# Performance work log

Hardware: AMD Instinct MI355X
Metric: run time of the kernel (lower is better)

The kernel has to match this reference:

```python
import jax, jax.numpy as jnp
import numpy as np

N_NODES_TOTAL = 61440   # B*30
NODES = 30              # per-graph node count (forced by view(-1, 30*128))
E = 491520
IN_CH = 12
CHANS = [128, 512, 128]
KSIZE = 3
FC_OUT = 72             # 12 * 6


def setup_inputs() -> dict:
    key = jax.random.key(0)
    ks = jax.random.split(key, 24)
    d = {}
    d['x'] = jax.random.normal(ks[0], (N_NODES_TOTAL, IN_CH), dtype=jnp.float32)
    d['edge_index'] = jax.random.randint(ks[1], (2, E), 0, N_NODES_TOTAL, dtype=jnp.int64)
    # GCNConv(12, 12): PyG Linear weight [out, in] + bias
    d['gcn_w'] = jax.random.normal(ks[2], (12, 12), dtype=jnp.float32) * (1.0 / np.sqrt(12))
    d['gcn_b'] = jnp.zeros((12,), dtype=jnp.float32)
    # TCN: 3 TemporalBlocks, each uses conv1 (k=3, dilated causal) + 1x1 downsample
    in_c = IN_CH
    for i, out_c in enumerate(CHANS):
        d[f'conv_w{i}'] = jax.random.normal(ks[3 + 4 * i], (out_c, in_c, KSIZE), dtype=jnp.float32) * 0.01
        d[f'conv_b{i}'] = jnp.zeros((out_c,), dtype=jnp.float32)
        d[f'down_w{i}'] = jax.random.normal(ks[4 + 4 * i], (out_c, in_c, 1), dtype=jnp.float32) * 0.01
        d[f'down_b{i}'] = jnp.zeros((out_c,), dtype=jnp.float32)
        in_c = out_c
    d['fc_w'] = jax.random.normal(ks[20], (FC_OUT, CHANS[-1] * NODES), dtype=jnp.float32) * (1.0 / np.sqrt(CHANS[-1] * NODES))
    d['fc_b'] = jnp.zeros((FC_OUT,), dtype=jnp.float32)
    return d


def gcn_conv(x, edge_index, w, b):
    # PyG GCNConv: h = x W^T, add self-loops, sym normalize, scatter-add, + bias
    n = x.shape[0]
    h = x @ w.T
    loop = jnp.arange(n, dtype=edge_index.dtype)
    src = jnp.concatenate([edge_index[0], loop])
    dst = jnp.concatenate([edge_index[1], loop])
    deg = jax.ops.segment_sum(jnp.ones(src.shape[0], dtype=h.dtype), dst, num_segments=n)
    dinv = jnp.where(deg > 0, jax.lax.rsqrt(deg), 0.0)
    norm = dinv[src] * dinv[dst]                       # [E+N]
    out = jax.ops.segment_sum(norm[:, None] * h[src], dst, num_segments=n)
    return out + b


def causal_conv1d(x, w, b, dilation):
    # torch Conv1d(pad=(k-1)*d both sides) + Chomp1d((k-1)*d) == left-pad causal conv
    k = w.shape[-1]
    pad = (k - 1) * dilation
    y = jax.lax.conv_general_dilated(
        x, w, window_strides=(1,), padding=[(pad, 0)],
        rhs_dilation=(dilation,), dimension_numbers=('NCH', 'OIH', 'NCH'))
    return y + b[None, :, None]


def reference(x, edge_index, gcn_w, gcn_b,
              conv_w0, conv_b0, down_w0, down_b0,
              conv_w1, conv_b1, down_w1, down_b1,
              conv_w2, conv_b2, down_w2, down_b2,
              fc_w, fc_b):
    X = gcn_conv(x, edge_index, gcn_w, gcn_b)          # [B*30, 12]
    X = X.reshape(-1, NODES, IN_CH).transpose(0, 2, 1)  # [B, 12, 30]
    blocks = [(conv_w0, conv_b0, down_w0, down_b0),
              (conv_w1, conv_b1, down_w1, down_b1),
              (conv_w2, conv_b2, down_w2, down_b2)]
    for i, (cw, cb, dw, db) in enumerate(blocks):
        dil = 3 ** i
        out = jax.nn.relu(causal_conv1d(X, cw, cb, dil))
        res = causal_conv1d(X, dw, db, 1)              # 1x1 downsample (always in!=out here)
        X = jax.nn.relu(out + res)
    T = jax.nn.relu(X)                                  # [B, 128, 30]
    T = T.reshape(T.shape[0], -1)                       # [B, 3840], channel-major like torch flatten
    return T @ fc_w.T + fc_b                            # [B, 72]
```

## Files before the change

kernel.cpp:

```cpp
#include <hip/hip_runtime.h>
#include <hip/hip_bf16.h>

#define N_NODES 61440
#define NEDGE   491520
#define BATCH   2048
#define TT      30
#define C1      128
#define C2      512
#define C3      128
#define FCK     3840
#define MAXDEG  40

typedef float floatx16 __attribute__((ext_vector_type(16)));
typedef __bf16 bfrag   __attribute__((ext_vector_type(8)));

static __device__ __forceinline__ unsigned short f2bf(float f) {
    unsigned u = __float_as_uint(f);
    u = u + 0x7fffu + ((u >> 16) & 1u);
    return (unsigned short)(u >> 16);
}
static __device__ __forceinline__ unsigned cvtpk(float lo, float hi) {
    unsigned r;
    asm("v_cvt_pk_bf16_f32 %0, %1, %2" : "=v"(r) : "v"(lo), "v"(hi));
    return r;
}
static __device__ __forceinline__ bfrag ldf(const void* p) { return *(const bfrag*)p; }
#define MFMA(a, b, c) __builtin_amdgcn_mfma_f32_32x32x16_bf16(a, b, c, 0, 0, 0)

__global__ void k_edges_repack(
        const int* __restrict__ e32, int* __restrict__ cnt,
        unsigned short* __restrict__ eidx,
        const float* __restrict__ cw0, const float* __restrict__ dw0,
        const float* __restrict__ cw1, const float* __restrict__ dw1,
        const float* __restrict__ cw2, const float* __restrict__ dw2,
        const float* __restrict__ fcw,
        float* __restrict__ w0T, float* __restrict__ d0T,
        unsigned short* __restrict__ W1f, unsigned short* __restrict__ D1f,
        unsigned short* __restrict__ W2f, unsigned short* __restrict__ D2f,
        unsigned short* __restrict__ FCWf) {
    if (blockIdx.x < 1920) {
        int i = blockIdx.x * 256 + threadIdx.x;
        bool is64 = (e32[1] == 0) & (e32[3] == 0) & (e32[5] == 0) & (e32[7] == 0);
        int s, d;
        if (is64) { s = e32[2 * i]; d = e32[2 * (NEDGE + i)]; }
        else      { s = e32[i];     d = e32[NEDGE + i]; }
        int slot = atomicAdd(&cnt[d], 1);
        if (slot < MAXDEG) eidx[slot * N_NODES + d] = (unsigned short)s;
        return;
    }
    int i = (blockIdx.x - 1920) * 256 + threadIdx.x;
    if (i < 36 * 128) { int oc = i & 127, r = i >> 7; w0T[i] = cw0[oc * 36 + r]; }
    if (i < 12 * 128) { int oc = i & 127, ic = i >> 7; d0T[i] = dw0[oc * 12 + ic]; }
    if (i < 196608) {
        int pos = i & 511, f = i >> 9;
        int lane = pos >> 3, e = pos & 7;
        int oct = f & 15, q = (f >> 4) & 7, tap = f >> 7;
        int oc = oct * 32 + (lane & 31), ic = q * 16 + (lane >> 5) * 8 + e;
        W1f[i] = f2bf(cw1[(oc * 128 + ic) * 3 + tap]);
    } else if (i < 262144) {
        int j = i - 196608;
        int pos = j & 511, f = j >> 9;
        int lane = pos >> 3, e = pos & 7;
        int oct = f & 15, q = f >> 4;
        int oc = oct * 32 + (lane & 31), ic = q * 16 + (lane >> 5) * 8 + e;
        D1f[j] = f2bf(dw1[oc * 128 + ic]);
    } else if (i < 458752) {
        int j = i - 262144;
        int pos = j & 511, f = j >> 9;
        int lane = pos >> 3, e = pos & 7;
        int oct = f & 3, q = (f >> 2) & 31, tap = f >> 7;
        int oc = oct * 32 + (lane & 31), ic = q * 16 + (lane >> 5) * 8 + e;
        W2f[j] = f2bf(cw2[(oc * 512 + ic) * 3 + tap]);
    } else if (i < 524288) {
        int j = i - 458752;
        int pos = j & 511, f = j >> 9;
        int lane = pos >> 3, e = pos & 7;
        int oct = f & 3, q = f >> 2;
        int oc = oct * 32 + (lane & 31), ic = q * 16 + (lane >> 5) * 8 + e;
        D2f[j] = f2bf(dw2[oc * 512 + ic]);
    } else if (i < 892928) {
        int j = i - 524288;
        int pos = j & 511, f = j >> 9;
        int lane = pos >> 3, e = pos & 7;
        int oct = f % 3, q = f / 3;
        int o = oct * 32 + (lane & 31);
        int k = q * 16 + (lane >> 5) * 8 + e;
        float v = (o < 72) ? fcw[o * 3840 + (k & 127) * 30 + (k >> 7)] : 0.f;
        FCWf[j] = f2bf(v);
    }
}

__global__ __launch_bounds__(256) void k_block0(
        const float* __restrict__ x, const int* __restrict__ cnt,
        const unsigned short* __restrict__ eidx,
        const float* __restrict__ gw, const float* __restrict__ gb,
        const float* __restrict__ w0T, const float* __restrict__ d0T,
        const float* __restrict__ cb0, const float* __restrict__ db0,
        unsigned short* __restrict__ X1b) {
    __shared__ float wl[36 * 128];
    __shared__ float dl[12 * 128];
    __shared__ float cbl[128], dbl[128];
    __shared__ float gwl[144], gbl[12];
    __shared__ float aL[120][12];
    __shared__ float x0[4 * TT * 12];
    __shared__ __align__(16) unsigned short st[2][TT * 136];
    int tid = threadIdx.x;
    int b0 = blockIdx.x * 4;
    for (int i = tid; i < 36 * 128; i += 256) wl[i] = w0T[i];
    for (int i = tid; i < 12 * 128; i += 256) dl[i] = d0T[i];
    if (tid < 128) { cbl[tid] = cb0[tid]; dbl[tid] = db0[tid]; }
    if (tid < 144) gwl[tid] = gw[tid];
    if (tid >= 144 && tid < 156) gbl[tid - 144] = gb[tid - 144];

    {
        int th = tid & 127;
        int grp = tid >> 7;
        if (th < 120) {
            size_t n = (size_t)b0 * TT + th;
            int ne = cnt[n]; if (ne > MAXDEG) ne = MAXDEG;
            float a0 = 0.f, a1 = 0.f, a2 = 0.f, a3 = 0.f, a4 = 0.f, a5 = 0.f;
            int j = 0;
            for (; j + 4 <= ne; j += 4) {
                int s0 = eidx[(j + 0) * N_NODES + n];
                int s1 = eidx[(j + 1) * N_NODES + n];
                int s2 = eidx[(j + 2) * N_NODES + n];
                int s3 = eidx[(j + 3) * N_NODES + n];
                float di0 = rsqrtf(1.0f + (float)cnt[s0]);
                float di1 = rsqrtf(1.0f + (float)cnt[s1]);
                float di2 = rsqrtf(1.0f + (float)cnt[s2]);
                float di3 = rsqrtf(1.0f + (float)cnt[s3]);
                const float2* xp0 = (const float2*)(x + (size_t)s0 * 12 + grp * 6);
                const float2* xp1 = (const float2*)(x + (size_t)s1 * 12 + grp * 6);
                const float2* xp2 = (const float2*)(x + (size_t)s2 * 12 + grp * 6);
                const float2* xp3 = (const float2*)(x + (size_t)s3 * 12 + grp * 6);
                float2 q00 = xp0[0], q01 = xp0[1], q02 = xp0[2];
                float2 q10 = xp1[0], q11 = xp1[1], q12 = xp1[2];
                float2 q20 = xp2[0], q21 = xp2[1], q22 = xp2[2];
                float2 q30 = xp3[0], q31 = xp3[1], q32 = xp3[2];
                a0 += di0 * q00.x; a1 += di0 * q00.y;
                a2 += di0 * q01.x; a3 += di0 * q01.y;
                a4 += di0 * q02.x; a5 += di0 * q02.y;
                a0 += di1 * q10.x; a1 += di1 * q10.y;
                a2 += di1 * q11.x; a3 += di1 * q11.y;
                a4 += di1 * q12.x; a5 += di1 * q12.y;
                a0 += di2 * q20.x; a1 += di2 * q20.y;
                a2 += di2 * q21.x; a3 += di2 * q21.y;
                a4 += di2 * q22.x; a5 += di2 * q22.y;
                a0 += di3 * q30.x; a1 += di3 * q30.y;
                a2 += di3 * q31.x; a3 += di3 * q31.y;
                a4 += di3 * q32.x; a5 += di3 * q32.y;
            }
            for (; j < ne; j++) {
                int s = eidx[j * N_NODES + n];
                float di = rsqrtf(1.0f + (float)cnt[s]);
                const float2* xp = (const float2*)(x + (size_t)s * 12 + grp * 6);
                float2 p0 = xp[0], p1 = xp[1], p2 = xp[2];
                a0 += di * p0.x; a1 += di * p0.y;
                a2 += di * p1.x; a3 += di * p1.y;
                a4 += di * p2.x; a5 += di * p2.y;
            }
            float* ap = &aL[th][grp * 6];
            ap[0] = a0; ap[1] = a1; ap[2] = a2; ap[3] = a3; ap[4] = a4; ap[5] = a5;
        }
    }
    __syncthreads();

    if (tid < 120) {
        size_t n = (size_t)b0 * TT + tid;
        float di = rsqrtf(1.0f + (float)cnt[n]);
        float d2 = di * di;
        const float4* xp = (const float4*)(x + n * 12);
        float u[12];
        #pragma unroll
        for (int q = 0; q < 3; q++) {
            float4 xv = xp[q];
            u[q*4+0] = di * aL[tid][q*4+0] + d2 * xv.x;
            u[q*4+1] = di * aL[tid][q*4+1] + d2 * xv.y;
            u[q*4+2] = di * aL[tid][q*4+2] + d2 * xv.z;
            u[q*4+3] = di * aL[tid][q*4+3] + d2 * xv.w;
        }
        #pragma unroll
        for (int c = 0; c < 12; c++) {
            float acc = gbl[c];
            #pragma unroll
            for (int j = 0; j < 12; j++) acc += u[j] * gwl[c * 12 + j];
            x0[tid * 12 + c] = acc;
        }
    }
    __syncthreads();

    int oc = tid & 127, half = tid >> 7;
    float cb = cbl[oc], db = dbl[oc];
    for (int bi = 0; bi < 2; bi++) {
        int bl = bi * 2 + half;
        const float* xb = x0 + bl * (TT * 12);
        float conv[TT], res[TT];
        #pragma unroll
        for (int t = 0; t < TT; t++) { conv[t] = 0.f; res[t] = 0.f; }
        #pragma unroll
        for (int ic = 0; ic < 12; ic++) {
            float w0v = wl[(ic * 3 + 0) * 128 + oc];
            float w1v = wl[(ic * 3 + 1) * 128 + oc];
            float w2v = wl[(ic * 3 + 2) * 128 + oc];
            float dv  = dl[ic * 128 + oc];
            #pragma unroll
            for (int t = 0; t < TT; t++) {
                float xv = xb[t * 12 + ic];
                conv[t] += w2v * xv;
                if (t + 1 < TT) conv[t + 1] += w1v * xv;
                if (t + 2 < TT) conv[t + 2] += w0v * xv;
                res[t] += dv * xv;
            }
        }
        #pragma unroll
        for (int t = 0; t < TT; t++) {
            float o1 = fmaxf(conv[t] + cb, 0.f);
            st[half][t * 136 + oc] = f2bf(fmaxf(o1 + res[t] + db, 0.f));
        }
        __syncthreads();
        for (int idx = tid; idx < 2 * TT * 16; idx += 256) {
            int h = idx / (TT * 16), rem = idx - h * (TT * 16);
            int row = rem >> 4, seg = rem & 15;
            *(uint4*)(X1b + (size_t)((b0 + bi * 2 + h) * TT + row) * 128 + seg * 8) =
                *(const uint4*)(&st[h][row * 136 + seg * 8]);
        }
        __syncthreads();
    }
}

__global__ __launch_bounds__(256, 2) void k_tcn12(
        const unsigned short* __restrict__ X1b,
        const unsigned short* __restrict__ W1f, const unsigned short* __restrict__ D1f,
        const float* __restrict__ cb1, const float* __restrict__ db1,
        const unsigned short* __restrict__ W2f, const unsigned short* __restrict__ D2f,
        const float* __restrict__ cb2, const float* __restrict__ db2,
        unsigned short* __restrict__ X3b) {
    __shared__ __align__(16) unsigned short X1l[61 * 136];
    __shared__ __align__(16) unsigned short X2l[61 * 520];
    const int tid  = threadIdx.x;
    const int lane = tid & 63;
    const int wave = tid >> 6;
    const int tcol = lane & 31;
    const int half = lane >> 5;
    const int b0 = blockIdx.x * 2;

    auto ldw1 = [&](bfrag* dst, int oct, int qc) {
        #pragma unroll
        for (int tap = 0; tap < 3; tap++)
            #pragma unroll
            for (int qq = 0; qq < 4; qq++)
                dst[tap * 4 + qq] =
                    ldf(W1f + (((tap * 8 + qc * 4 + qq) * 16 + oct) << 9) + lane * 8);
        #pragma unroll
        for (int qq = 0; qq < 4; qq++)
            dst[12 + qq] = ldf(D1f + (((qc * 4 + qq) * 16 + oct) << 9) + lane * 8);
    };
    auto ldw2 = [&](bfrag* dst, int oct, int qc) {
        #pragma unroll
        for (int tap = 0; tap < 3; tap++)
            #pragma unroll
            for (int qq = 0; qq < 4; qq++)
                dst[tap * 4 + qq] =
                    ldf(W2f + (((tap * 32 + qc * 4 + qq) * 4 + oct) << 9) + lane * 8);
        #pragma unroll
        for (int qq = 0; qq < 4; qq++)
            dst[12 + qq] = ldf(D2f + (((qc * 4 + qq) * 4 + oct) << 9) + lane * 8);
    };

    bfrag wf[2][16];
    ldw1(wf[0], wave, 0);

    for (int idx = tid; idx < 960; idx += 256) {
        int row = idx >> 4, seg = idx & 15;
        *(uint4*)(X1l + row * 136 + seg * 8) =
            *(const uint4*)(X1b + ((size_t)(b0 * 30 + row) << 7) + seg * 8);
    }
    if (tid < 17) *(uint4*)(X1l + 60 * 136 + tid * 8) = make_uint4(0, 0, 0, 0);
    if (tid < 65) *(uint4*)(X2l + 60 * 520 + tid * 8) = make_uint4(0, 0, 0, 0);
    __syncthreads();

    {
        floatx16 accc[2], accd[2];
        #pragma unroll
        for (int s = 0; s < 8; s++) {
            const int qc = s & 1;
            const int oct = (s >> 1) * 4 + wave;
            if (qc == 0) {
                #pragma unroll
                for (int gi = 0; gi < 4; gi++) {
                    int ocb = oct * 32 + half * 4 + gi * 8;
                    float4 cbv = *(const float4*)(cb1 + ocb);
                    float4 dbv = *(const float4*)(db1 + ocb);
                    accc[0][gi*4+0] = cbv.x; accc[0][gi*4+1] = cbv.y;
                    accc[0][gi*4+2] = cbv.z; accc[0][gi*4+3] = cbv.w;
                    accd[0][gi*4+0] = dbv.x; accd[0][gi*4+1] = dbv.y;
                    accd[0][gi*4+2] = dbv.z; accd[0][gi*4+3] = dbv.w;
                    accc[1][gi*4+0] = cbv.x; accc[1][gi*4+1] = cbv.y;
                    accc[1][gi*4+2] = cbv.z; accc[1][gi*4+3] = cbv.w;
                    accd[1][gi*4+0] = dbv.x; accd[1][gi*4+1] = dbv.y;
                    accd[1][gi*4+2] = dbv.z; accd[1][gi*4+3] = dbv.w;
                }
            }
            if (s < 7)
                ldw1(wf[(s + 1) & 1], ((s + 1) >> 1) * 4 + wave, (s + 1) & 1);
            #pragma unroll
            for (int bl = 0; bl < 2; bl++) {
                bfrag bx[3][4];
                #pragma unroll
                for (int si = 0; si < 3; si++) {
                    int trow = tcol - si * 3;
                    const unsigned short* rp = ((unsigned)trow < 30u)
                        ? (X1l + (bl * 30 + trow) * 136) : (X1l + 60 * 136);
                    #pragma unroll
                    for (int qq = 0; qq < 4; qq++)
                        bx[si][qq] = ldf(rp + (qc * 4 + qq) * 16 + half * 8);
                }
                #pragma unroll
                for (int qq = 0; qq < 4; qq++) {
                    accc[bl] = MFMA(wf[s & 1][8 + qq],  bx[0][qq], accc[bl]);
                    accc[bl] = MFMA(wf[s & 1][4 + qq],  bx[1][qq], accc[bl]);
                    accc[bl] = MFMA(wf[s & 1][qq],      bx[2][qq], accc[bl]);
                    accd[bl] = MFMA(wf[s & 1][12 + qq], bx[0][qq], accd[bl]);
                }
            }
            if (qc == 1 && tcol < 30) {
                #pragma unroll
                for (int bl = 0; bl < 2; bl++) {
                    unsigned short* wp = X2l + (bl * 30 + tcol) * 520 + oct * 32 + half * 4;
                    #pragma unroll
                    for (int gi = 0; gi < 4; gi++) {
                        float v0 = fmaxf(fmaxf(accc[bl][gi*4+0], 0.f) + accd[bl][gi*4+0], 0.f);
                        float v1 = fmaxf(fmaxf(accc[bl][gi*4+1], 0.f) + accd[bl][gi*4+1], 0.f);
                        float v2 = fmaxf(fmaxf(accc[bl][gi*4+2], 0.f) + accd[bl][gi*4+2], 0.f);
                        float v3 = fmaxf(fmaxf(accc[bl][gi*4+3], 0.f) + accd[bl][gi*4+3], 0.f);
                        *(uint2*)(wp + gi * 8) = make_uint2(cvtpk(v0, v1), cvtpk(v2, v3));
                    }
                }
            }
        }
    }
    bfrag wf2[2][16];
    ldw2(wf2[0], wave, 0);
    __syncthreads();

    {
        const int oct = wave;
        floatx16 accc[2], accd[2];
        #pragma unroll
        for (int gi = 0; gi < 4; gi++) {
            int ocb = oct * 32 + half * 4 + gi * 8;
            float4 cbv = *(const float4*)(cb2 + ocb);
            float4 dbv = *(const float4*)(db2 + ocb);
            accc[0][gi*4+0] = cbv.x; accc[0][gi*4+1] = cbv.y;
            accc[0][gi*4+2] = cbv.z; accc[0][gi*4+3] = cbv.w;
            accd[0][gi*4+0] = dbv.x; accd[0][gi*4+1] = dbv.y;
            accd[0][gi*4+2] = dbv.z; accd[0][gi*4+3] = dbv.w;
            accc[1][gi*4+0] = cbv.x; accc[1][gi*4+1] = cbv.y;
            accc[1][gi*4+2] = cbv.z; accc[1][gi*4+3] = cbv.w;
            accd[1][gi*4+0] = dbv.x; accd[1][gi*4+1] = dbv.y;
            accd[1][gi*4+2] = dbv.z; accd[1][gi*4+3] = dbv.w;
        }
        #pragma unroll
        for (int qc = 0; qc < 8; qc++) {
            if (qc < 7) ldw2(wf2[(qc + 1) & 1], oct, qc + 1);
            #pragma unroll
            for (int bl = 0; bl < 2; bl++) {
                bfrag bx[3][4];
                #pragma unroll
                for (int si = 0; si < 3; si++) {
                    int trow = tcol - si * 9;
                    const unsigned short* rp = ((unsigned)trow < 30u)
                        ? (X2l + (bl * 30 + trow) * 520) : (X2l + 60 * 520);
                    #pragma unroll
                    for (int qq = 0; qq < 4; qq++)
                        bx[si][qq] = ldf(rp + (qc * 4 + qq) * 16 + half * 8);
                }
                #pragma unroll
                for (int qq = 0; qq < 4; qq++) {
                    accc[bl] = MFMA(wf2[qc & 1][8 + qq],  bx[0][qq], accc[bl]);
                    accc[bl] = MFMA(wf2[qc & 1][4 + qq],  bx[1][qq], accc[bl]);
                    accc[bl] = MFMA(wf2[qc & 1][qq],      bx[2][qq], accc[bl]);
                    accd[bl] = MFMA(wf2[qc & 1][12 + qq], bx[0][qq], accd[bl]);
                }
            }
        }
        if (tcol < 30) {
            #pragma unroll
            for (int bl = 0; bl < 2; bl++) {
                unsigned short* wp = X1l + (bl * 30 + tcol) * 136 + oct * 32 + half * 4;
                #pragma unroll
                for (int gi = 0; gi < 4; gi++) {
                    float v0 = fmaxf(fmaxf(accc[bl][gi*4+0], 0.f) + accd[bl][gi*4+0], 0.f);
                    float v1 = fmaxf(fmaxf(accc[bl][gi*4+1], 0.f) + accd[bl][gi*4+1], 0.f);
                    float v2 = fmaxf(fmaxf(accc[bl][gi*4+2], 0.f) + accd[bl][gi*4+2], 0.f);
                    float v3 = fmaxf(fmaxf(accc[bl][gi*4+3], 0.f) + accd[bl][gi*4+3], 0.f);
                    *(uint2*)(wp + gi * 8) = make_uint2(cvtpk(v0, v1), cvtpk(v2, v3));
                }
            }
        }
    }
    __syncthreads();
    for (int idx = tid; idx < 960; idx += 256) {
        int row = idx >> 4, seg = idx & 15;
        *(uint4*)(X3b + ((size_t)(b0 * 30 + row) << 7) + seg * 8) =
            *(const uint4*)(X1l + row * 136 + seg * 8);
    }
}

__global__ __launch_bounds__(256) void k_fc_mfma(
        const unsigned short* __restrict__ X3b,
        const unsigned short* __restrict__ FCWf,
        unsigned short* __restrict__ P) {
    __shared__ __align__(16) unsigned short xt[128 * 248];
    const int tid  = threadIdx.x;
    const int lane = tid & 63;
    const int wave = tid >> 6;
    const int half = lane >> 5;
    const int bg = blockIdx.x & 15;
    const int kc = blockIdx.x >> 4;

    for (int idx = tid; idx < 128 * 32; idx += 256) {
        int row = idx >> 5, seg = idx & 31;
        if (seg < 30)
            *(uint4*)(xt + row * 248 + seg * 8) =
                *(const uint4*)(X3b + (size_t)(bg * 128 + row) * FCK + kc * 240 + seg * 8);
    }
    __syncthreads();

    const int bl = wave * 32 + (lane & 31);
    floatx16 acc[3];
    acc[0] = 0; acc[1] = 0; acc[2] = 0;
    #pragma unroll
    for (int ql = 0; ql < 15; ql++) {
        int q = kc * 15 + ql;
        bfrag bx = ldf(xt + bl * 248 + ql * 16 + half * 8);
        #pragma unroll
        for (int oct = 0; oct < 3; oct++) {
            bfrag af = ldf(FCWf + ((q * 3 + oct) << 9) + lane * 8);
            acc[oct] = MFMA(af, bx, acc[oct]);
        }
    }
    unsigned short* base = P + (size_t)kc * 96 * BATCH;
    const int b = bg * 128 + bl;
    #pragma unroll
    for (int oct = 0; oct < 3; oct++)
        #pragma unroll
        for (int j = 0; j < 16; j++) {
            int o = oct * 32 + half * 4 + (j >> 2) * 8 + (j & 3);
            base[(size_t)o * BATCH + b] = f2bf(acc[oct][j]);
        }
}

__global__ __launch_bounds__(256) void k_fc_reduce(
        const unsigned short* __restrict__ P, const float* __restrict__ fcb,
        float* __restrict__ out) {
    int j = blockIdx.x * blockDim.x + threadIdx.x;
    int o = j >> 11, b = j & 2047;
    float acc = fcb[o];
    #pragma unroll
    for (int kc = 0; kc < 16; kc++) {
        unsigned u = P[((size_t)kc * 96 + o) * BATCH + b];
        acc += __uint_as_float(u << 16);
    }
    out[b * 72 + o] = acc;
}


extern "C" void kernel_launch(void* const* d_in, const int* in_sizes, int n_in,
                              void* d_out, int out_size, void* d_ws, size_t ws_size,
                              hipStream_t stream) {
    const float* x   = (const float*)d_in[0];
    const int*   e32 = (const int*)  d_in[1];
    const float* gw  = (const float*)d_in[2];
    const float* gb  = (const float*)d_in[3];
    const float* cw0 = (const float*)d_in[4];
    const float* cb0 = (const float*)d_in[5];
    const float* dw0 = (const float*)d_in[6];
    const float* db0 = (const float*)d_in[7];
    const float* cw1 = (const float*)d_in[8];
    const float* cb1 = (const float*)d_in[9];
    const float* dw1 = (const float*)d_in[10];
    const float* db1 = (const float*)d_in[11];
    const float* cw2 = (const float*)d_in[12];
    const float* cb2 = (const float*)d_in[13];
    const float* dw2 = (const float*)d_in[14];
    const float* db2 = (const float*)d_in[15];
    const float* fcw = (const float*)d_in[16];
    const float* fcb = (const float*)d_in[17];

    char* w = (char*)d_ws;
    auto alloc = [&](size_t bytes) {
        char* p = w;
        w += (bytes + 255) & ~(size_t)255;
        return p;
    };
    int*            cnt  = (int*)           alloc(N_NODES * 4);
    unsigned short* eidx = (unsigned short*)alloc((size_t)N_NODES * MAXDEG * 2);
    float* w0T  = (float*)alloc(36 * 128 * 4);
    float* d0T  = (float*)alloc(12 * 128 * 4);
    unsigned short* W1f  = (unsigned short*)alloc(196608 * 2);
    unsigned short* D1f  = (unsigned short*)alloc(65536 * 2);
    unsigned short* W2f  = (unsigned short*)alloc(196608 * 2);
    unsigned short* D2f  = (unsigned short*)alloc(65536 * 2);
    unsigned short* FCWf = (unsigned short*)alloc(368640 * 2);
    unsigned short* X1b  = (unsigned short*)alloc((size_t)BATCH * TT * C1 * 2);
    unsigned short* X3b  = (unsigned short*)alloc((size_t)BATCH * TT * C3 * 2);
    unsigned short* P    = (unsigned short*)alloc((size_t)16 * 96 * BATCH * 2);

    hipMemsetAsync(cnt, 0, N_NODES * 4, stream);
    k_edges_repack<<<1920 + 3488, 256, 0, stream>>>(
        e32, cnt, eidx, cw0, dw0, cw1, dw1, cw2, dw2, fcw,
        w0T, d0T, W1f, D1f, W2f, D2f, FCWf);
    k_block0<<<BATCH / 4, 256, 0, stream>>>(x, cnt, eidx, gw, gb,
                                            w0T, d0T, cb0, db0, X1b);
    k_tcn12<<<BATCH / 2, 256, 0, stream>>>(X1b, W1f, D1f, cb1, db1,
                                           W2f, D2f, cb2, db2, X3b);
    k_fc_mfma<<<256, 256, 0, stream>>>(X3b, FCWf, P);
    k_fc_reduce<<<72 * BATCH / 256, 256, 0, stream>>>(P, fcb, (float*)d_out);
}
```

Before: 151.1 us.

## Fuse GCN and TCN block0 into the block1-2 MFMA kernel

Merges the GCN aggregation and first temporal block into the kernel that runs blocks 1 and 2. Block0 output goes straight into shared memory instead of being written to and reloaded from a global bf16 buffer. Block0 scratch is aliased onto the X2 shared buffer. This removes one kernel launch and the X1 global round trip. In exchange, each block now handles 2 graphs rather than 4 for the GCN stage, so those threads are less occupied, and the scalar block0 work runs under the two-blocks-per-CU launch bound.

```diff
diff --git a/kernel.cpp b/kernel.cpp
--- a/kernel.cpp
+++ b/kernel.cpp
@@ -90,22 +90,35 @@
     }
 }
 
-__global__ __launch_bounds__(256) void k_block0(
+__global__ __launch_bounds__(256, 2) void k_tcn012(
         const float* __restrict__ x, const int* __restrict__ cnt,
         const unsigned short* __restrict__ eidx,
         const float* __restrict__ gw, const float* __restrict__ gb,
         const float* __restrict__ w0T, const float* __restrict__ d0T,
         const float* __restrict__ cb0, const float* __restrict__ db0,
-        unsigned short* __restrict__ X1b) {
-    __shared__ float wl[36 * 128];
-    __shared__ float dl[12 * 128];
-    __shared__ float cbl[128], dbl[128];
-    __shared__ float gwl[144], gbl[12];
-    __shared__ float aL[120][12];
-    __shared__ float x0[4 * TT * 12];
-    __shared__ __align__(16) unsigned short st[2][TT * 136];
-    int tid = threadIdx.x;
-    int b0 = blockIdx.x * 4;
+        const unsigned short* __restrict__ W1f, const unsigned short* __restrict__ D1f,
+        const float* __restrict__ cb1, const float* __restrict__ db1,
+        const unsigned short* __restrict__ W2f, const unsigned short* __restrict__ D2f,
+        const float* __restrict__ cb2, const float* __restrict__ db2,
+        unsigned short* __restrict__ X3b) {
+    __shared__ __align__(16) unsigned short X1l[61 * 136];
+    __shared__ __align__(16) unsigned short X2l[61 * 520];
+    const int tid  = threadIdx.x;
+    const int lane = tid & 63;
+    const int wave = tid >> 6;
+    const int tcol = lane & 31;
+    const int half = lane >> 5;
+    const int b0 = blockIdx.x * 2;
+
+    float* wl  = (float*)X2l;
+    float* dl  = wl + 36 * 128;
+    float* cbl = dl + 12 * 128;
+    float* dbl = cbl + 128;
+    float* gwl = dbl + 128;
+    float* gbl = gwl + 144;
+    float* aL  = gbl + 12;
+    float* x0  = aL + 720;
+
     for (int i = tid; i < 36 * 128; i += 256) wl[i] = w0T[i];
     for (int i = tid; i < 12 * 128; i += 256) dl[i] = d0T[i];
     if (tid < 128) { cbl[tid] = cb0[tid]; dbl[tid] = db0[tid]; }
@@ -115,7 +128,7 @@
     {
         int th = tid & 127;
         int grp = tid >> 7;
-        if (th < 120) {
+        if (th < 60) {
             size_t n = (size_t)b0 * TT + th;
             int ne = cnt[n]; if (ne > MAXDEG) ne = MAXDEG;
             float a0 = 0.f, a1 = 0.f, a2 = 0.f, a3 = 0.f, a4 = 0.f, a5 = 0.f;
@@ -159,13 +172,13 @@
                 a2 += di * p1.x; a3 += di * p1.y;
                 a4 += di * p2.x; a5 += di * p2.y;
             }
-            float* ap = &aL[th][grp * 6];
+            float* ap = aL + th * 12 + grp * 6;
             ap[0] = a0; ap[1] = a1; ap[2] = a2; ap[3] = a3; ap[4] = a4; ap[5] = a5;
         }
     }
     __syncthreads();
 
-    if (tid < 120) {
+    if (tid < 60) {
         size_t n = (size_t)b0 * TT + tid;
         float di = rsqrtf(1.0f + (float)cnt[n]);
         float d2 = di * di;
@@ -174,10 +187,10 @@
         #pragma unroll
         for (int q = 0; q < 3; q++) {
             float4 xv = xp[q];
-            u[q*4+0] = di * aL[tid][q*4+0] + d2 * xv.x;
-            u[q*4+1] = di * aL[tid][q*4+1] + d2 * xv.y;
-            u[q*4+2] = di * aL[tid][q*4+2] + d2 * xv.z;
-            u[q*4+3] = di * aL[tid][q*4+3] + d2 * xv.w;
+            u[q*4+0] = di * aL[tid * 12 + q*4+0] + d2 * xv.x;
+            u[q*4+1] = di * aL[tid * 12 + q*4+1] + d2 * xv.y;
+            u[q*4+2] = di * aL[tid * 12 + q*4+2] + d2 * xv.z;
+            u[q*4+3] = di * aL[tid * 12 + q*4+3] + d2 * xv.w;
         }
         #pragma unroll
         for (int c = 0; c < 12; c++) {
@@ -189,10 +202,9 @@
     }
     __syncthreads();
 
-    int oc = tid & 127, half = tid >> 7;
-    float cb = cbl[oc], db = dbl[oc];
-    for (int bi = 0; bi < 2; bi++) {
-        int bl = bi * 2 + half;
+    {
+        int oc = tid & 127, bl = tid >> 7;
+        float cb = cbl[oc], db = dbl[oc];
         const float* xb = x0 + bl * (TT * 12);
         float conv[TT], res[TT];
         #pragma unroll
@@ -215,34 +227,11 @@
         #pragma unroll
         for (int t = 0; t < TT; t++) {
             float o1 = fmaxf(conv[t] + cb, 0.f);
-            st[half][t * 136 + oc] = f2bf(fmaxf(o1 + res[t] + db, 0.f));
-        }
-        __syncthreads();
-        for (int idx = tid; idx < 2 * TT * 16; idx += 256) {
-            int h = idx / (TT * 16), rem = idx - h * (TT * 16);
-            int row = rem >> 4, seg = rem & 15;
-            *(uint4*)(X1b + (size_t)((b0 + bi * 2 + h) * TT + row) * 128 + seg * 8) =
-                *(const uint4*)(&st[h][row * 136 + seg * 8]);
-        }
-        __syncthreads();
-    }
-}
-
-__global__ __launch_bounds__(256, 2) void k_tcn12(
-        const unsigned short* __restrict__ X1b,
-        const unsigned short* __restrict__ W1f, const unsigned short* __restrict__ D1f,
-        const float* __restrict__ cb1, const float* __restrict__ db1,
-        const unsigned short* __restrict__ W2f, const unsigned short* __restrict__ D2f,
-        const float* __restrict__ cb2, const float* __restrict__ db2,
-        unsigned short* __restrict__ X3b) {
-    __shared__ __align__(16) unsigned short X1l[61 * 136];
-    __shared__ __align__(16) unsigned short X2l[61 * 520];
-    const int tid  = threadIdx.x;
-    const int lane = tid & 63;
-    const int wave = tid >> 6;
-    const int tcol = lane & 31;
-    const int half = lane >> 5;
-    const int b0 = blockIdx.x * 2;
+            X1l[(bl * 30 + t) * 136 + oc] = f2bf(fmaxf(o1 + res[t] + db, 0.f));
+        }
+    }
+    if (tid < 17) *(uint4*)(X1l + 60 * 136 + tid * 8) = make_uint4(0, 0, 0, 0);
+    if (tid < 65) *(uint4*)(X2l + 60 * 520 + tid * 8) = make_uint4(0, 0, 0, 0);
 
     auto ldw1 = [&](bfrag* dst, int oct, int qc) {
         #pragma unroll
@@ -269,14 +258,6 @@
 
     bfrag wf[2][16];
     ldw1(wf[0], wave, 0);
-
-    for (int idx = tid; idx < 960; idx += 256) {
-        int row = idx >> 4, seg = idx & 15;
-        *(uint4*)(X1l + row * 136 + seg * 8) =
-            *(const uint4*)(X1b + ((size_t)(b0 * 30 + row) << 7) + seg * 8);
-    }
-    if (tid < 17) *(uint4*)(X1l + 60 * 136 + tid * 8) = make_uint4(0, 0, 0, 0);
-    if (tid < 65) *(uint4*)(X2l + 60 * 520 + tid * 8) = make_uint4(0, 0, 0, 0);
     __syncthreads();
 
     {
@@ -503,7 +484,6 @@
     unsigned short* W2f  = (unsigned short*)alloc(196608 * 2);
     unsigned short* D2f  = (unsigned short*)alloc(65536 * 2);
     unsigned short* FCWf = (unsigned short*)alloc(368640 * 2);
-    unsigned short* X1b  = (unsigned short*)alloc((size_t)BATCH * TT * C1 * 2);
     unsigned short* X3b  = (unsigned short*)alloc((size_t)BATCH * TT * C3 * 2);
     unsigned short* P    = (unsigned short*)alloc((size_t)16 * 96 * BATCH * 2);
 
@@ -511,10 +491,9 @@
     k_edges_repack<<<1920 + 3488, 256, 0, stream>>>(
         e32, cnt, eidx, cw0, dw0, cw1, dw1, cw2, dw2, fcw,
         w0T, d0T, W1f, D1f, W2f, D2f, FCWf);
-    k_block0<<<BATCH / 4, 256, 0, stream>>>(x, cnt, eidx, gw, gb,
-                                            w0T, d0T, cb0, db0, X1b);
-    k_tcn12<<<BATCH / 2, 256, 0, stream>>>(X1b, W1f, D1f, cb1, db1,
-                                           W2f, D2f, cb2, db2, X3b);
+    k_tcn012<<<BATCH / 2, 256, 0, stream>>>(
+        x, cnt, eidx, gw, gb, w0T, d0T, cb0, db0,
+        W1f, D1f, cb1, db1, W2f, D2f, cb2, db2, X3b);
     k_fc_mfma<<<256, 256, 0, stream>>>(X3b, FCWf, P);
     k_fc_reduce<<<72 * BATCH / 256, 256, 0, stream>>>(P, fcb, (float*)d_out);
 }
```

After: 144.3 us. 4.5% less time.
